# Optimization experiments

Measured on AMD Instinct MI355X. Metric: run time of the kernel, lower is better.

Reference implementation:

```python
import jax, jax.numpy as jnp
import numpy as np

NUM_COMPONENTS = 8
STRIDE, PADDING, OUTPUT_PADDING, K = 2, 1, 0, 4


def get_comp_mat(n):
    # Cayley-Dickson construction: entry [i, j] = +/- component index of the
    # weight multiplying input component j to produce output component i.
    A = np.array([[0]])
    while A.shape[0] < n:
        m = A.shape[0]
        A = np.vstack([np.hstack([A, -(A + m)]), np.hstack([A + m, A])])
    return A


def setup_inputs() -> dict:
    key = jax.random.key(0)
    k1, k2, k3 = jax.random.split(key, 3)
    B, Cin, Cout, H = 8, 512, 256, 64
    c_in, c_out = Cin // NUM_COMPONENTS, Cout // NUM_COMPONENTS
    x = jax.random.normal(k1, (B, Cin, H, H), jnp.float32)
    # per-component ConvTranspose2d weights, torch layout [C_in, C_out, kH, kW]
    W = jax.random.normal(k2, (NUM_COMPONENTS, c_in, c_out, K, K), jnp.float32) * 0.05
    b = jax.random.normal(k3, (NUM_COMPONENTS, c_out), jnp.float32) * 0.05
    return {"x": x, "W": W, "b": b}


def reference(x, W, b):
    n = NUM_COMPONENTS
    comp = get_comp_mat(n)                 # static [n, n] signed component table
    signs = jnp.asarray(np.where(comp < 0, -1.0, 1.0), x.dtype)
    idx = np.abs(comp)                     # which sub-conv weight to use
    c_in, c_out, kh, kw = W.shape[1:]
    # Fuse the n^2 transpose convs into ONE block transpose conv:
    # Kbig[j*c_in:(j+1)*c_in, i*c_out:(i+1)*c_out] = sign[i,j] * W[idx[i,j]]
    Wsel = W[idx] * signs[:, :, None, None, None, None]          # [ni, nj, c_in, c_out, kh, kw]
    Wbig = jnp.transpose(Wsel, (1, 2, 0, 3, 4, 5)).reshape(n * c_in, n * c_out, kh, kw)
    bbig = jnp.einsum('ij,ijc->ic', signs, b[idx]).reshape(n * c_out)
    # torch ConvTranspose2d == conv with input dilated by stride and flipped kernel
    rhs = jnp.flip(Wbig, (2, 3)).transpose(1, 0, 2, 3)           # OIHW
    pad = K - 1 - PADDING
    out = jax.lax.conv_general_dilated(
        x, rhs, window_strides=(1, 1),
        padding=((pad, pad + OUTPUT_PADDING), (pad, pad + OUTPUT_PADDING)),
        lhs_dilation=(STRIDE, STRIDE),
        dimension_numbers=('NCHW', 'OIHW', 'NCHW'))
    return out + bbig[None, :, None, None]
```

## Files before the change

### kernel.cpp

```cpp
#include <hip/hip_runtime.h>
#include <hip/hip_bf16.h>

typedef unsigned short ushort_t;
typedef __attribute__((ext_vector_type(8))) short short8;
typedef __attribute__((ext_vector_type(4))) float f32x4;

#define NCOMP    8
#define CIN      512
#define COUT     256
#define H        64
#define HP       66
#define OHW      128
#define NB       8

__device__ const int d_idx8[8][8] = {
    {0,1,2,1,4,3,2,3},
    {1,0,3,2,5,4,1,2},
    {2,1,0,1,6,5,4,3},
    {3,2,1,0,7,6,5,4},
    {4,3,2,3,0,1,2,1},
    {5,4,1,2,1,0,3,2},
    {6,5,4,3,2,1,0,1},
    {7,6,5,4,3,2,1,0}};

__device__ const int kh_tab[2][2] = {{1,3},{0,2}};
__device__ const int dh_tab[2][2] = {{0,-1},{1,0}};

__global__ void prep_x(const float* __restrict__ x, ushort_t* __restrict__ xpadT) {
    __shared__ ushort_t tile[32][33];
    const int ih  = blockIdx.x;
    const int iw0 = (blockIdx.y & 1) * 32;
    const int ic0 = (blockIdx.y >> 1) * 32;
    const int b   = blockIdx.z;
    const int t   = threadIdx.x;

    for (int e = t; e < 1024; e += 256) {
        int icl = e >> 5, iwl = e & 31;
        float v = x[(((size_t)b * CIN + ic0 + icl) * H + ih) * H + iw0 + iwl];
        __hip_bfloat16 h = __float2bfloat16(v);
        tile[icl][iwl] = *(ushort_t*)&h;
    }
    __syncthreads();
    const int iwl = t >> 3, g = t & 7;
    ushort4 v;
    v.x = tile[g * 4 + 0][iwl];
    v.y = tile[g * 4 + 1][iwl];
    v.z = tile[g * 4 + 2][iwl];
    v.w = tile[g * 4 + 3][iwl];
    ushort_t* dst = xpadT + (((size_t)b * HP + ih + 1) * HP + iw0 + iwl + 1) * CIN + ic0 + g * 4;
    *(ushort4*)dst = v;
}

__global__ void prep_w(const float* __restrict__ W, const float* __restrict__ bias,
                       ushort_t* __restrict__ Abf, float* __restrict__ bbig) {
    const int t = blockIdx.x * blockDim.x + threadIdx.x;
    if (t < 4 * 64 * 256 * 32) {
        int kin = t & 31;
        int oc  = (t >> 5) & 255;
        int ks  = (t >> 13) & 63;
        int cls = t >> 19;
        int k  = ks * 32 + kin;
        int a  = k >> 10, c = (k >> 9) & 1, ic = k & 511;
        int ph = cls >> 1, pw = cls & 1;
        int kh = kh_tab[ph][a], kw = kh_tab[pw][c];
        int i = oc >> 5, co = oc & 31;
        int j = ic >> 6, ci = ic & 63;
        float s = (i >= j) ? 1.0f : -1.0f;
        float v = s * W[(((size_t)(d_idx8[i][j] * 64 + ci) * 32 + co) * 4 + kh) * 4 + kw];
        __hip_bfloat16 h = __float2bfloat16(v);
        Abf[t] = *(ushort_t*)&h;
    }
    if (t < COUT) {
        int i = t >> 5, co = t & 31;
        float acc = 0.0f;
        for (int j = 0; j < NCOMP; ++j)
            acc += ((i >= j) ? 1.0f : -1.0f) * bias[d_idx8[i][j] * 32 + co];
        bbig[t] = acc;
    }
}

__device__ __forceinline__ void async16(void* lds_dst, const void* g_src) {
    __builtin_amdgcn_global_load_lds(
        (const __attribute__((address_space(1))) unsigned int*)g_src,
        (__attribute__((address_space(3))) unsigned int*)lds_dst,
        16, 0, 0);
}

__launch_bounds__(256)
__global__ void htconv_mfma(const ushort_t* __restrict__ xpadT,
                            const ushort_t* __restrict__ Abf,
                            const float* __restrict__ bbig,
                            float* __restrict__ out) {
    __shared__ __align__(16) ushort_t smem[8192];
    char* sb = (char*)smem;

    const int t     = threadIdx.x;
    const int ntile = blockIdx.x;
    const int mtile = blockIdx.y;
    const int cls   = blockIdx.z & 3;
    const int b     = blockIdx.z >> 2;
    const int ph = cls >> 1, pw = cls & 1;
    const int ohh0 = ntile * 2;

    const int srcc = (((t & 3) ^ ((t >> 3) & 3)) * 8);
    const int m_a  = t >> 2;
    const ushort_t* ap = Abf + (((size_t)cls * 64) * 256 + (size_t)mtile * 128 + m_a) * 32 + srcc;

    const int dh0 = dh_tab[ph][0], dh1 = dh_tab[ph][1];
    const int dw0 = dh_tab[pw][0], dw1 = dh_tab[pw][1];
    const int oww = t >> 2;
    const ushort_t* bp[2][2][2];
#pragma unroll
    for (int a = 0; a < 2; ++a) {
        int dh = (a == 0) ? dh0 : dh1;
#pragma unroll
        for (int c = 0; c < 2; ++c) {
            int dw = (c == 0) ? dw0 : dw1;
#pragma unroll
            for (int row = 0; row < 2; ++row) {
                size_t idx = (((size_t)b * HP + ohh0 + row + dh + 1) * HP + oww + dw + 1) * CIN + srcc;
                bp[a][c][row] = xpadT + idx;
            }
        }
    }

    const int lane = t & 63, wave = t >> 6;
    const int wm = wave >> 1, wn = wave & 1;
    const int col = lane & 15, quad = lane >> 4;
    const int soff = (quad ^ ((col >> 1) & 3)) * 16;
    const int aoff = (wm * 64 + col) * 64 + soff;
    const int boff = 8192 + (wn * 64 + col) * 64 + soff;

    f32x4 acc[4][4];
#pragma unroll
    for (int i = 0; i < 4; ++i)
#pragma unroll
        for (int j = 0; j < 4; ++j)
            acc[i][j] = (f32x4){0.f, 0.f, 0.f, 0.f};

#pragma unroll
    for (int a = 0; a < 2; ++a) {
#pragma unroll
        for (int c = 0; c < 2; ++c) {
            const ushort_t* b0 = bp[a][c][0];
            const ushort_t* b1 = bp[a][c][1];
            for (int kk = 0; kk < 16; ++kk) {
                async16(sb + t * 16,         ap);
                async16(sb + 4096 + t * 16,  ap + 2048);
                async16(sb + 8192 + t * 16,  b0);
                async16(sb + 12288 + t * 16, b1);
                ap += 8192; b0 += 32; b1 += 32;
                __syncthreads();

                short8 af[4], bf[4];
#pragma unroll
                for (int s = 0; s < 4; ++s) {
                    af[s] = *(const short8*)(sb + aoff + s * 1024);
                    bf[s] = *(const short8*)(sb + boff + s * 1024);
                }
#pragma unroll
                for (int sm = 0; sm < 4; ++sm)
#pragma unroll
                    for (int sn = 0; sn < 4; ++sn)
                        acc[sm][sn] = __builtin_amdgcn_mfma_f32_16x16x32_bf16(
                            af[sm], bf[sn], acc[sm][sn], 0, 0, 0);
                __syncthreads();
            }
        }
    }

    const int oh = 2 * (ohh0 + wn) + ph;
#pragma unroll
    for (int sm = 0; sm < 4; ++sm) {
#pragma unroll
        for (int r = 0; r < 4; ++r) {
            const int occ = mtile * 128 + wm * 64 + sm * 16 + quad * 4 + r;
            const float bv = bbig[occ];
            float* obase = out + (((size_t)b * COUT + occ) * OHW + oh) * OHW + pw;
#pragma unroll
            for (int sn = 0; sn < 4; ++sn) {
                const int owi = sn * 16 + col;
                obase[2 * owi] = acc[sm][sn][r] + bv;
            }
        }
    }
}

extern "C" void kernel_launch(void* const* d_in, const int* in_sizes, int n_in,
                              void* d_out, int out_size, void* d_ws, size_t ws_size,
                              hipStream_t stream) {
    const float* x    = (const float*)d_in[0];
    const float* W    = (const float*)d_in[1];
    const float* bias = (const float*)d_in[2];
    float* out = (float*)d_out;

    ushort_t* xpadT = (ushort_t*)d_ws;
    ushort_t* Abf   = xpadT + (size_t)NB * HP * HP * CIN;
    float*    bbig  = (float*)(Abf + (size_t)4 * 64 * 256 * 32);

    hipMemsetAsync(xpadT, 0, (size_t)NB * HP * HP * CIN * sizeof(ushort_t), stream);
    prep_x<<<dim3(H, 32, NB), 256, 0, stream>>>(x, xpadT);
    prep_w<<<dim3((4 * 64 * 256 * 32) / 256), 256, 0, stream>>>(W, bias, Abf, bbig);
    htconv_mfma<<<dim3(32, 2, 32), 256, 0, stream>>>(xpadT, Abf, bbig, out);
}
```

Measured before the change: 372.2 us.

## Use channel-group planar bf16 input layout and fuse prep kernels into one launch

Reorganizes the padded bf16 input into per-batch planes of 8-channel groups so each GEMM k-step reads contiguous 16-byte pixel chunks across adjacent columns. The full-buffer memset is replaced with border-only zeroing, and the x, weight and bias preparation kernels are merged into a single launch. This reduces launch count and memset traffic, at the cost of a larger per-k-step stride between planes in the conv loop.

```diff
diff --git a/kernel.cpp b/kernel.cpp
--- a/kernel.cpp
+++ b/kernel.cpp
@@ -10,6 +10,9 @@
 #define COUT     256
 #define H        64
 #define HP       66
+#define PLANE    (HP * HP)
+#define PLANE_EL (PLANE * 8)
+#define KSTRIDE  (4 * PLANE_EL)
 #define OHW      128
 #define NB       8
 
@@ -26,39 +29,60 @@
 __device__ const int kh_tab[2][2] = {{1,3},{0,2}};
 __device__ const int dh_tab[2][2] = {{0,-1},{1,0}};
 
-__global__ void prep_x(const float* __restrict__ x, ushort_t* __restrict__ xpadT) {
-    __shared__ ushort_t tile[32][33];
-    const int ih  = blockIdx.x;
-    const int iw0 = (blockIdx.y & 1) * 32;
-    const int ic0 = (blockIdx.y >> 1) * 32;
-    const int b   = blockIdx.z;
-    const int t   = threadIdx.x;
-
-    for (int e = t; e < 1024; e += 256) {
-        int icl = e >> 5, iwl = e & 31;
-        float v = x[(((size_t)b * CIN + ic0 + icl) * H + ih) * H + iw0 + iwl];
-        __hip_bfloat16 h = __float2bfloat16(v);
-        tile[icl][iwl] = *(ushort_t*)&h;
-    }
-    __syncthreads();
-    const int iwl = t >> 3, g = t & 7;
-    ushort4 v;
-    v.x = tile[g * 4 + 0][iwl];
-    v.y = tile[g * 4 + 1][iwl];
-    v.z = tile[g * 4 + 2][iwl];
-    v.w = tile[g * 4 + 3][iwl];
-    ushort_t* dst = xpadT + (((size_t)b * HP + ih + 1) * HP + iw0 + iwl + 1) * CIN + ic0 + g * 4;
-    *(ushort4*)dst = v;
-}
-
-__global__ void prep_w(const float* __restrict__ W, const float* __restrict__ bias,
-                       ushort_t* __restrict__ Abf, float* __restrict__ bbig) {
-    const int t = blockIdx.x * blockDim.x + threadIdx.x;
-    if (t < 4 * 64 * 256 * 32) {
-        int kin = t & 31;
-        int oc  = (t >> 5) & 255;
-        int ks  = (t >> 13) & 63;
-        int cls = t >> 19;
+__global__ void prep_all(const float* __restrict__ x, const float* __restrict__ W,
+                         const float* __restrict__ bias,
+                         ushort_t* __restrict__ xpadT, ushort_t* __restrict__ Abf,
+                         float* __restrict__ bbig) {
+    __shared__ ushort_t tile[64 * 66];
+    const int q = blockIdx.x;
+    const int t = threadIdx.x;
+
+    if (q < 4096) {
+        const int b   = q & 7;
+        const int ih  = (q >> 3) & 63;
+        const int ccg = q >> 9;
+#pragma unroll
+        for (int i = 0; i < 16; ++i) {
+            int e = i * 256 + t;
+            int ic_l = e >> 6, iw = e & 63;
+            float v = x[(((size_t)b * CIN + ccg * 64 + ic_l) * H + ih) * H + iw];
+            __hip_bfloat16 h = __float2bfloat16(v);
+            tile[ic_l * 66 + iw] = *(ushort_t*)&h;
+        }
+        __syncthreads();
+#pragma unroll
+        for (int r = 0; r < 2; ++r) {
+            int q2 = r * 256 + t;
+            int cc_l = q2 >> 6, iw = q2 & 63;
+            ushort_t us[8];
+#pragma unroll
+            for (int j = 0; j < 8; ++j) us[j] = tile[(cc_l * 8 + j) * 66 + iw];
+            uint4 v;
+            v.x = (unsigned)us[0] | ((unsigned)us[1] << 16);
+            v.y = (unsigned)us[2] | ((unsigned)us[3] << 16);
+            v.z = (unsigned)us[4] | ((unsigned)us[5] << 16);
+            v.w = (unsigned)us[6] | ((unsigned)us[7] << 16);
+            ushort_t* dst = xpadT + ((size_t)(b * 64 + ccg * 8 + cc_l) * PLANE
+                                     + (ih + 1) * HP + (iw + 1)) * 8;
+            *(uint4*)dst = v;
+        }
+    } else if (q < 4608) {
+        const int p = q - 4096;
+        ushort_t* base = xpadT + (size_t)p * PLANE_EL;
+        if (t < 260) {
+            int ihp, iwp;
+            if      (t < 66)  { ihp = 0;           iwp = t; }
+            else if (t < 132) { ihp = HP - 1;      iwp = t - 66; }
+            else if (t < 196) { ihp = t - 132 + 1; iwp = 0; }
+            else              { ihp = t - 196 + 1; iwp = HP - 1; }
+            *(uint4*)(base + (ihp * HP + iwp) * 8) = make_uint4(0, 0, 0, 0);
+        }
+    } else if (q < 12800) {
+        const int gid = (q - 4608) * 256 + t;
+        int kin = gid & 31;
+        int oc  = (gid >> 5) & 255;
+        int ks  = (gid >> 13) & 63;
+        int cls = gid >> 19;
         int k  = ks * 32 + kin;
         int a  = k >> 10, c = (k >> 9) & 1, ic = k & 511;
         int ph = cls >> 1, pw = cls & 1;
@@ -68,14 +92,15 @@
         float s = (i >= j) ? 1.0f : -1.0f;
         float v = s * W[(((size_t)(d_idx8[i][j] * 64 + ci) * 32 + co) * 4 + kh) * 4 + kw];
         __hip_bfloat16 h = __float2bfloat16(v);
-        Abf[t] = *(ushort_t*)&h;
-    }
-    if (t < COUT) {
-        int i = t >> 5, co = t & 31;
-        float acc = 0.0f;
-        for (int j = 0; j < NCOMP; ++j)
-            acc += ((i >= j) ? 1.0f : -1.0f) * bias[d_idx8[i][j] * 32 + co];
-        bbig[t] = acc;
+        Abf[gid] = *(ushort_t*)&h;
+    } else {
+        if (t < COUT) {
+            int i = t >> 5, co = t & 31;
+            float acc = 0.0f;
+            for (int j = 0; j < NCOMP; ++j)
+                acc += ((i >= j) ? 1.0f : -1.0f) * bias[d_idx8[i][j] * 32 + co];
+            bbig[t] = acc;
+        }
     }
 }
 
@@ -102,9 +127,9 @@
     const int ph = cls >> 1, pw = cls & 1;
     const int ohh0 = ntile * 2;
 
-    const int srcc = (((t & 3) ^ ((t >> 3) & 3)) * 8);
+    const int swz  = (t & 3) ^ ((t >> 3) & 3);
     const int m_a  = t >> 2;
-    const ushort_t* ap = Abf + (((size_t)cls * 64) * 256 + (size_t)mtile * 128 + m_a) * 32 + srcc;
+    const ushort_t* ap = Abf + (((size_t)cls * 64) * 256 + (size_t)mtile * 128 + m_a) * 32 + swz * 8;
 
     const int dh0 = dh_tab[ph][0], dh1 = dh_tab[ph][1];
     const int dw0 = dh_tab[pw][0], dw1 = dh_tab[pw][1];
@@ -118,7 +143,8 @@
             int dw = (c == 0) ? dw0 : dw1;
 #pragma unroll
             for (int row = 0; row < 2; ++row) {
-                size_t idx = (((size_t)b * HP + ohh0 + row + dh + 1) * HP + oww + dw + 1) * CIN + srcc;
+                size_t idx = ((size_t)(b * 64 + swz) * PLANE
+                              + (ohh0 + row + dh + 1) * HP + (oww + dw + 1)) * 8;
                 bp[a][c][row] = xpadT + idx;
             }
         }
@@ -149,7 +175,7 @@
                 async16(sb + 4096 + t * 16,  ap + 2048);
                 async16(sb + 8192 + t * 16,  b0);
                 async16(sb + 12288 + t * 16, b1);
-                ap += 8192; b0 += 32; b1 += 32;
+                ap += 8192; b0 += KSTRIDE; b1 += KSTRIDE;
                 __syncthreads();
 
                 short8 af[4], bf[4];
@@ -195,11 +221,10 @@
     float* out = (float*)d_out;
 
     ushort_t* xpadT = (ushort_t*)d_ws;
-    ushort_t* Abf   = xpadT + (size_t)NB * HP * HP * CIN;
-    float*    bbig  = (float*)(Abf + (size_t)4 * 64 * 256 * 32);
-
-    hipMemsetAsync(xpadT, 0, (size_t)NB * HP * HP * CIN * sizeof(ushort_t), stream);
-    prep_x<<<dim3(H, 32, NB), 256, 0, stream>>>(x, xpadT);
-    prep_w<<<dim3((4 * 64 * 256 * 32) / 256), 256, 0, stream>>>(W, bias, Abf, bbig);
+    ushort_t* Abf   = xpadT + (size_t)NB * 64 * PLANE_EL / 8;
+    Abf = xpadT + (size_t)NB * 64 * PLANE * 8;
+    float* bbig = (float*)(Abf + (size_t)4 * 64 * 256 * 32);
+
+    prep_all<<<dim3(12801), 256, 0, stream>>>(x, W, bias, xpadT, Abf, bbig);
     htconv_mfma<<<dim3(32, 2, 32), 256, 0, stream>>>(xpadT, Abf, bbig, out);
 }
```

Measured after the change: 372.6 us. No clear change (+0.1%).
